# Kernel tuning notes

Measured on AMD Instinct MI355X. Metric: run time of the kernel, lower is better.

## Reference

```python
import jax, jax.numpy as jnp
import numpy as np

B, C, H, W, E, HEADS = 8, 128, 96, 96, 16, 4
HD = C // HEADS

def _ln(x, g, b, eps=1e-5):
    m = jnp.mean(x, axis=-1, keepdims=True)
    v = jnp.mean(jnp.square(x - m), axis=-1, keepdims=True)
    return (x - m) * jax.lax.rsqrt(v + eps) * g + b

def _gelu(x):
    return jax.nn.gelu(x, approximate=False)  # torch nn.GELU default (erf)

def setup_inputs() -> dict:
    key = jax.random.key(0)
    ks = iter(jax.random.split(key, 48))
    def wgt(shape, s=0.02):
        return jax.random.normal(next(ks), shape, jnp.float32) * s
    d = {
        "feature_map": jax.random.normal(next(ks), (B, C, H, W), jnp.float32),
        "hyperedge_scores": jax.random.uniform(next(ks), (B, H * W, E), jnp.float32),
        # norm_node_pre
        "np_g": jnp.ones((C,), jnp.float32), "np_b": jnp.zeros((C,), jnp.float32),
        # MultiheadAttention (self-attn over hyperedges)
        "mha_w_in": wgt((3 * C, C)), "mha_b_in": jnp.zeros((3 * C,), jnp.float32),
        "mha_w_out": wgt((C, C)), "mha_b_out": jnp.zeros((C,), jnp.float32),
        # transformer FFN
        "ffn_w1": wgt((2 * C, C)), "ffn_b1": jnp.zeros((2 * C,), jnp.float32),
        "ffn_w2": wgt((C, 2 * C)), "ffn_b2": jnp.zeros((C,), jnp.float32),
        # shared LayerNorm inside HypergraphTransformerConv (used twice)
        "tnorm_g": jnp.ones((C,), jnp.float32), "tnorm_b": jnp.zeros((C,), jnp.float32),
        # norm_hyper
        "nh_g": jnp.ones((C,), jnp.float32), "nh_b": jnp.zeros((C,), jnp.float32),
        # hyper_proj
        "hp_w": wgt((C, C)), "hp_b": jnp.zeros((C,), jnp.float32),
        # HyperedgeGuidedNodeAttention
        "q_w": wgt((C, C)), "q_b": jnp.zeros((C,), jnp.float32),
        "kv_w": wgt((2 * C, C)), "kv_b": jnp.zeros((2 * C,), jnp.float32),
        # norm_fusion
        "nf_g": jnp.ones((2 * C,), jnp.float32), "nf_b": jnp.zeros((2 * C,), jnp.float32),
        # gate = Linear(2C->C) + LayerNorm(C) + Sigmoid
        "gate_w": wgt((C, 2 * C)), "gate_b": jnp.zeros((C,), jnp.float32),
        "gate_ln_g": jnp.ones((C,), jnp.float32), "gate_ln_b": jnp.zeros((C,), jnp.float32),
        # node_proj
        "nproj_w": wgt((C, C)), "nproj_b": jnp.zeros((C,), jnp.float32),
    }
    return d

def _forward(feature_map, hyperedge_scores, np_g, np_b, mha_w_in, mha_b_in,
             mha_w_out, mha_b_out, ffn_w1, ffn_b1, ffn_w2, ffn_b2,
             tnorm_g, tnorm_b, nh_g, nh_b, hp_w, hp_b, q_w, q_b, kv_w, kv_b,
             nf_g, nf_b, gate_w, gate_b, gate_ln_g, gate_ln_b, nproj_w, nproj_b):
    b, c, h, w = feature_map.shape
    n = h * w
    node = jnp.transpose(feature_map.reshape(b, c, n), (0, 2, 1))   # [B,N,C]
    node = _ln(node, np_g, np_b)
    # hyperedge aggregation: H^T @ X -> [B,E,C]
    hyper = jnp.einsum('bne,bnc->bec', hyperedge_scores, node)
    # --- HypergraphTransformerConv (self-attn over E=16 hyperedges) ---
    qkv = hyper @ mha_w_in.T + mha_b_in                               # [B,E,3C]
    q, k, v = jnp.split(qkv, 3, axis=-1)
    def heads(x):  # [B,E,C] -> [B,h,E,hd]
        return jnp.transpose(x.reshape(b, E, HEADS, HD), (0, 2, 1, 3))
    q, k, v = heads(q), heads(k), heads(v)
    attn = jax.nn.softmax(jnp.einsum('bhqd,bhkd->bhqk', q, k) / np.sqrt(HD), axis=-1)
    ao = jnp.einsum('bhqk,bhkd->bhqd', attn, v)
    ao = jnp.transpose(ao, (0, 2, 1, 3)).reshape(b, E, c)
    ao = ao @ mha_w_out.T + mha_b_out
    x = _ln(hyper + ao, tnorm_g, tnorm_b)
    ffn = _gelu(x @ ffn_w1.T + ffn_b1) @ ffn_w2.T + ffn_b2
    hyper = _ln(x + ffn, tnorm_g, tnorm_b)
    # ---
    hyper = _ln(hyper, nh_g, nh_b)
    hyper = _gelu(hyper @ hp_w.T + hp_b)                              # [B,E,C]
    intra = jnp.einsum('bne,bec->bnc', hyperedge_scores, hyper)       # [B,N,C]
    # HyperedgeGuidedNodeAttention (scale = C**-0.5)
    Q = node @ q_w.T + q_b
    K, V = jnp.split(hyper @ kv_w.T + kv_b, 2, axis=-1)
    a = jax.nn.softmax(jnp.einsum('bnc,bec->bne', Q, K) * (c ** -0.5), axis=-1)
    cross = jnp.einsum('bne,bec->bnc', a, V)
    combined = _ln(jnp.concatenate([intra, cross], axis=-1), nf_g, nf_b)
    gate = jax.nn.sigmoid(_ln(combined @ gate_w.T + gate_b, gate_ln_g, gate_ln_b))
    fused = gate * intra + (1.0 - gate) * cross
    upd = node + fused                                                # dropout in eval mode
    out = _gelu(upd @ nproj_w.T + nproj_b)
    return jnp.transpose(out, (0, 2, 1)).reshape(b, c, h, w)

def reference(feature_map, hyperedge_scores, np_g, np_b, mha_w_in, mha_b_in,
              mha_w_out, mha_b_out, ffn_w1, ffn_b1, ffn_w2, ffn_b2,
              tnorm_g, tnorm_b, nh_g, nh_b, hp_w, hp_b, q_w, q_b, kv_w, kv_b,
              nf_g, nf_b, gate_w, gate_b, gate_ln_g, gate_ln_b, nproj_w, nproj_b):
    return _forward(feature_map, hyperedge_scores, np_g, np_b, mha_w_in, mha_b_in,
                    mha_w_out, mha_b_out, ffn_w1, ffn_b1, ffn_w2, ffn_b2,
                    tnorm_g, tnorm_b, nh_g, nh_b, hp_w, hp_b, q_w, q_b, kv_w, kv_b,
                    nf_g, nf_b, gate_w, gate_b, gate_ln_g, gate_ln_b, nproj_w, nproj_b)
```

## Files before the change

### kernel.cpp

```cpp
#include <hip/hip_runtime.h>

typedef unsigned short bf_t;
typedef unsigned int u32;
typedef short short8 __attribute__((ext_vector_type(8)));
typedef float f32x4 __attribute__((ext_vector_type(4)));

#define NB 8
#define CC 128
#define NN 9216
#define EE 16
#define NT 144
#define HS 24

__device__ __forceinline__ float b2f(bf_t u){ return __uint_as_float(((u32)u)<<16); }
__device__ __forceinline__ bf_t f2b(float f){
  u32 u = __float_as_uint(f);
  u = (u + 0x7fffu + ((u>>16)&1u)) >> 16;
  return (bf_t)u;
}
__device__ __forceinline__ float gelu_f(float x){ return 0.5f*x*(1.f+erff(x*0.70710678118654752f)); }
__device__ __forceinline__ float red16(float v){
  #pragma unroll
  for (int m=1;m<16;m<<=1) v += __shfl_xor(v, m, 16);
  return v;
}
__device__ __forceinline__ float grs(float var){
  return rsqrtf(fmaxf(var + 1e-5f, 1e-8f));
}
__device__ __forceinline__ short8 ldw8(const float* __restrict__ p){
  float4 a = *(const float4*)p;
  float4 b = *(const float4*)(p+4);
  short8 o;
  o[0]=(short)f2b(a.x); o[1]=(short)f2b(a.y); o[2]=(short)f2b(a.z); o[3]=(short)f2b(a.w);
  o[4]=(short)f2b(b.x); o[5]=(short)f2b(b.y); o[6]=(short)f2b(b.z); o[7]=(short)f2b(b.w);
  return o;
}

template<int MODE>
__global__ __launch_bounds__(256) void k_pre(float* __restrict__ hacc,
    const float* __restrict__ gw, const float* __restrict__ npw,
    bf_t* __restrict__ gwb, bf_t* __restrict__ npwb,
    const float* __restrict__ w_in, const float* __restrict__ w_out,
    const float* __restrict__ w1, const float* __restrict__ w2,
    const float* __restrict__ hpw, const float* __restrict__ kvw,
    const float* __restrict__ qw,
    bf_t* __restrict__ w_in_b, bf_t* __restrict__ w_out_b,
    bf_t* __restrict__ w1_b, bf_t* __restrict__ w2_b,
    bf_t* __restrict__ hpw_b, bf_t* __restrict__ kvw_b,
    bf_t* __restrict__ qwT_b){
  int i = blockIdx.x*256 + threadIdx.x;
  hacc[i] = 0.f;
  if (MODE >= 1){
    gwb[i]       = f2b(gw[i]);
    gwb[i+16384] = f2b(gw[i+16384]);
    npwb[i]      = f2b(npw[i]);
  }
  if (MODE == 2){
    #pragma unroll
    for (int k=0;k<3;k++) w_in_b[i + k*16384] = f2b(w_in[i + k*16384]);
    w_out_b[i]       = f2b(w_out[i]);
    w1_b[i]          = f2b(w1[i]);
    w1_b[i+16384]    = f2b(w1[i+16384]);
    w2_b[i]          = f2b(w2[i]);
    w2_b[i+16384]    = f2b(w2[i+16384]);
    hpw_b[i]         = f2b(hpw[i]);
    kvw_b[i]         = f2b(kvw[i]);
    kvw_b[i+16384]   = f2b(kvw[i+16384]);
    qwT_b[i]         = f2b(qw[(i&127)*128 + (i>>7)]);
  }
}

template<int BFOUT>
__global__ __launch_bounds__(256,4) void k_ln_agg(const float* __restrict__ fm,
                                                  const float* __restrict__ g,
                                                  const float* __restrict__ bb,
                                                  const float* __restrict__ sc,
                                                  float* __restrict__ nln,
                                                  bf_t* __restrict__ nlnb,
                                                  float* __restrict__ hacc){
  int b = blockIdx.y, n0 = blockIdx.x*64, tid = threadIdx.x;
  __shared__ float xs[128*65];
  __shared__ float scs[64][17];
  __shared__ float ps[4][64], pq[4][64], mrs[2][64];
  const float* base = fm + (size_t)b*CC*NN + n0;
  #pragma unroll
  for (int p=0;p<8;p++){
    int idx = tid + p*256;
    int c = idx>>4, n4 = (idx&15)*4;
    float4 v = *(const float4*)(base + (size_t)c*NN + n4);
    xs[c*65 + n4+0] = v.x; xs[c*65 + n4+1] = v.y;
    xs[c*65 + n4+2] = v.z; xs[c*65 + n4+3] = v.w;
  }
  { int n = tid>>2, e4 = (tid&3)*4;
    float4 sv = *(const float4*)(sc + ((size_t)(b*NN + n0 + n))*EE + e4);
    scs[n][e4+0] = sv.x; scs[n][e4+1] = sv.y;
    scs[n][e4+2] = sv.z; scs[n][e4+3] = sv.w;
  }
  __syncthreads();
  { int cg = tid>>6, n = tid&63;
    float s=0.f, q=0.f;
    #pragma unroll
    for (int c=0;c<32;c++){ float v = xs[(cg*32+c)*65 + n]; s+=v; q+=v*v; }
    ps[cg][n]=s; pq[cg][n]=q;
  }
  __syncthreads();
  if (tid < 64){
    float S = ps[0][tid]+ps[1][tid]+ps[2][tid]+ps[3][tid];
    float Q = pq[0][tid]+pq[1][tid]+pq[2][tid]+pq[3][tid];
    float m = S*(1.f/128.f);
    mrs[0][tid] = m; mrs[1][tid] = grs(Q*(1.f/128.f) - m*m);
  }
  __syncthreads();
  #pragma unroll
  for (int p=0;p<8;p++){
    int idx = tid + p*256;
    int c = idx>>4, n4 = (idx&15)*4;
    float gv = g[c], bv = bb[c];
    float v0 = (xs[c*65+n4+0]-mrs[0][n4+0])*mrs[1][n4+0]*gv + bv;
    float v1 = (xs[c*65+n4+1]-mrs[0][n4+1])*mrs[1][n4+1]*gv + bv;
    float v2 = (xs[c*65+n4+2]-mrs[0][n4+2])*mrs[1][n4+2]*gv + bv;
    float v3 = (xs[c*65+n4+3]-mrs[0][n4+3])*mrs[1][n4+3]*gv + bv;
    xs[c*65+n4+0]=v0; xs[c*65+n4+1]=v1; xs[c*65+n4+2]=v2; xs[c*65+n4+3]=v3;
    if (!BFOUT){
      float4 o; o.x=v0; o.y=v1; o.z=v2; o.w=v3;
      *(float4*)(nln + ((size_t)(b*CC + c))*NN + n0 + n4) = o;
    }
  }
  __syncthreads();
  if (BFOUT){
    #pragma unroll
    for (int p=0;p<4;p++){
      int idx = tid + p*256;
      int n = idx>>4, c8 = (idx&15)*8;
      short8 o;
      #pragma unroll
      for (int j=0;j<8;j++) o[j] = (short)f2b(xs[(c8+j)*65 + n]);
      *(short8*)(nlnb + ((size_t)(b*NN + n0 + n))*CC + c8) = o;
    }
  }
  { int cp = tid&63, eh = tid>>6;
    float a0[4]={0,0,0,0}, a1[4]={0,0,0,0};
    for (int n=0;n<64;n++){
      float x0 = xs[cp*65 + n], x1 = xs[(cp+64)*65 + n];
      #pragma unroll
      for (int j=0;j<4;j++){
        float se = scs[n][eh*4+j];
        a0[j] += se*x0; a1[j] += se*x1;
      }
    }
    #pragma unroll
    for (int j=0;j<4;j++){
      float* hb = hacc + (size_t)(b*EE + eh*4 + j)*CC;
      atomicAdd(hb + cp, a0[j]);
      atomicAdd(hb + cp + 64, a1[j]);
    }
  }
}

template<int K, int NOUT, int ACT, int WB, int NW>
__device__ __forceinline__ void gemm16(const bf_t* A, int SA,
                                       const float* __restrict__ W,
                                       const bf_t* __restrict__ Wb,
                                       const float* __restrict__ bias,
                                       bf_t* O, int SO, int tid){
  int lane = tid&63, wid = tid>>6;
  int m16 = lane&15, quad = lane>>4;
  for (int t0 = wid; t0 < NOUT/16; t0 += NW){
    int n0 = t0*16;
    f32x4 acc = {0.f,0.f,0.f,0.f};
    #pragma unroll
    for (int k0=0;k0<K;k0+=32){
      short8 af = *(const short8*)(A + m16*SA + k0 + quad*8);
      short8 bfv = WB ? *(const short8*)(Wb + (size_t)(n0+m16)*K + k0 + quad*8)
                      : ldw8(W + (size_t)(n0+m16)*K + k0 + quad*8);
      acc = __builtin_amdgcn_mfma_f32_16x16x32_bf16(af, bfv, acc, 0, 0, 0);
    }
    int col = n0 + m16;
    float bv = bias[col];
    #pragma unroll
    for (int r=0;r<4;r++){
      float v = acc[r] + bv;
      if (ACT) v = gelu_f(v);
      O[(quad*4+r)*SO + col] = f2b(v);
    }
  }
}

#define SP1 136
#define SP2 264
#define SP3 392

template<int WB>
__global__ __launch_bounds__(512) void k_edge(const float* __restrict__ hacc,
    const float* w_in, const float* b_in, const float* w_out, const float* b_out,
    const float* w1, const float* b1, const float* w2, const float* b2v,
    const float* tg, const float* tb, const float* nhg, const float* nhb,
    const float* hpw, const float* hpb, const float* kvw, const float* kvbias,
    const float* qw, const float* qb,
    const bf_t* __restrict__ w_in_b, const bf_t* __restrict__ w_out_b,
    const bf_t* __restrict__ w1_b, const bf_t* __restrict__ w2_b,
    const bf_t* __restrict__ hpw_b, const bf_t* __restrict__ kvw_b,
    const bf_t* __restrict__ qwT_b,
    bf_t* __restrict__ hfw, bf_t* __restrict__ vws,
    bf_t* __restrict__ Ktgb, float* __restrict__ qbK){
  __shared__ __align__(16) bf_t hyp0[16*SP1];
  __shared__ __align__(16) bf_t qkvb[16*SP3];
  __shared__ __align__(16) bf_t aob [16*SP1];
  __shared__ __align__(16) bf_t xnb [16*SP1];
  __shared__ __align__(16) bf_t h1b [16*SP2];
  __shared__ __align__(16) bf_t t2b [16*SP1];
  __shared__ __align__(16) bf_t hfb [16*SP1];
  __shared__ __align__(16) bf_t kvo [16*SP2];
  int b = blockIdx.x, tid = threadIdx.x;
  int lane = tid&63, wid = tid>>6, m16 = lane&15, quad = lane>>4;

  #pragma unroll
  for (int p=0;p<4;p++){
    int idx = tid + p*512;
    int e = idx>>7, c = idx&127;
    hyp0[e*SP1 + c] = f2b(hacc[(size_t)(b*EE + e)*CC + c]);
  }
  __syncthreads();
  gemm16<128,384,0,WB,8>(hyp0, SP1, w_in, w_in_b, b_in, qkvb, SP3, tid);
  __syncthreads();
  if (tid < 256){
    int part = tid&3, hq = tid>>2;
    int h = hq>>4, qi = hq&15;
    int dbase = h*32 + part*8;
    float qv[8];
    #pragma unroll
    for (int j=0;j<8;j++) qv[j] = b2f(qkvb[qi*SP3 + dbase + j]);
    float dot[16];
    #pragma unroll
    for (int kk=0;kk<16;kk++){
      float s = 0.f;
      #pragma unroll
      for (int j=0;j<8;j++) s += qv[j]*b2f(qkvb[kk*SP3 + 128 + dbase + j]);
      dot[kk] = s;
    }
    #pragma unroll
    for (int m=1;m<4;m<<=1){
      #pragma unroll
      for (int kk=0;kk<16;kk++) dot[kk] += __shfl_xor(dot[kk], m, 4);
    }
    const float sc1 = 0.17677669529663687f;
    float mx = -1e30f;
    #pragma unroll
    for (int kk=0;kk<16;kk++){ dot[kk] *= sc1; mx = fmaxf(mx, dot[kk]); }
    float sum = 0.f;
    #pragma unroll
    for (int kk=0;kk<16;kk++){ dot[kk] = __expf(dot[kk]-mx); sum += dot[kk]; }
    float inv = 1.f/sum;
    float ao[8] = {0,0,0,0,0,0,0,0};
    #pragma unroll
    for (int kk=0;kk<16;kk++){
      float p = dot[kk]*inv;
      #pragma unroll
      for (int j=0;j<8;j++) ao[j] += p*b2f(qkvb[kk*SP3 + 256 + dbase + j]);
    }
    #pragma unroll
    for (int j=0;j<8;j++) aob[qi*SP1 + dbase + j] = f2b(ao[j]);
  }
  __syncthreads();
  gemm16<128,128,0,WB,8>(aob, SP1, w_out, w_out_b, b_out, xnb, SP1, tid);
  __syncthreads();
  if (tid < 256){
    int e = tid>>4, i = tid&15;
    float v[8]; float s=0.f, q=0.f;
    #pragma unroll
    for (int j=0;j<8;j++){
      int c = i*8+j;
      v[j] = b2f(hyp0[e*SP1+c]) + b2f(xnb[e*SP1+c]);
      s += v[j]; q += v[j]*v[j];
    }
    s = red16(s); q = red16(q);
    float m = s*(1.f/128.f);
    float rs = grs(q*(1.f/128.f) - m*m);
    #pragma unroll
    for (int j=0;j<8;j++){
      int c = i*8+j;
      xnb[e*SP1+c] = f2b((v[j]-m)*rs*tg[c] + tb[c]);
    }
  }
  __syncthreads();
  gemm16<128,256,1,WB,8>(xnb, SP1, w1, w1_b, b1, h1b, SP2, tid);
  __syncthreads();
  gemm16<256,128,0,WB,8>(h1b, SP2, w2, w2_b, b2v, aob, SP1, tid);
  __syncthreads();
  if (tid < 256){
    int e = tid>>4, i = tid&15;
    float v[8]; float s=0.f, q=0.f;
    #pragma unroll
    for (int j=0;j<8;j++){
      int c = i*8+j;
      v[j] = b2f(xnb[e*SP1+c]) + b2f(aob[e*SP1+c]);
      s += v[j]; q += v[j]*v[j];
    }
    s = red16(s); q = red16(q);
    float m = s*(1.f/128.f);
    float rs = grs(q*(1.f/128.f) - m*m);
    float s2=0.f, q2=0.f;
    #pragma unroll
    for (int j=0;j<8;j++){
      int c = i*8+j;
      v[j] = (v[j]-m)*rs*tg[c] + tb[c];
      s2 += v[j]; q2 += v[j]*v[j];
    }
    s2 = red16(s2); q2 = red16(q2);
    float m2 = s2*(1.f/128.f);
    float rs2 = grs(q2*(1.f/128.f) - m2*m2);
    #pragma unroll
    for (int j=0;j<8;j++){
      int c = i*8+j;
      t2b[e*SP1+c] = f2b((v[j]-m2)*rs2*nhg[c] + nhb[c]);
    }
  }
  __syncthreads();
  gemm16<128,128,1,WB,8>(t2b, SP1, hpw, hpw_b, hpb, hfb, SP1, tid);
  __syncthreads();
  gemm16<128,256,0,WB,8>(hfb, SP1, kvw, kvw_b, kvbias, kvo, SP2, tid);
  __syncthreads();
  #pragma unroll
  for (int p=0;p<4;p++){
    int idx = tid + p*512;
    int e = idx>>7, c = idx&127;
    size_t o = (size_t)(b*EE + e)*CC + c;
    hfw[o] = hfb[e*SP1 + c];
    vws[o] = kvo[e*SP2 + 128 + c];
  }
  {
    int n0 = wid*16;
    f32x4 acc = {0.f,0.f,0.f,0.f};
    #pragma unroll
    for (int k0=0;k0<128;k0+=32){
      short8 a = *(const short8*)(kvo + m16*SP2 + k0 + quad*8);
      short8 bq;
      if (WB){
        bq = *(const short8*)(qwT_b + (size_t)(n0+m16)*128 + k0 + quad*8);
      } else {
        #pragma unroll
        for (int j=0;j<8;j++)
          bq[j] = (short)f2b(qw[(size_t)(k0+quad*8+j)*128 + n0+m16]);
      }
      acc = __builtin_amdgcn_mfma_f32_16x16x32_bf16(a, bq, acc, 0, 0, 0);
    }
    #pragma unroll
    for (int r=0;r<4;r++)
      Ktgb[(size_t)(b*EE + quad*4 + r)*CC + n0 + m16] = f2b(acc[r]);
  }
  if (tid < 256){
    int e = tid>>4, i = tid&15;
    float s = 0.f;
    #pragma unroll
    for (int j=0;j<8;j++) s += qb[i*8+j]*b2f(kvo[e*SP2 + i*8+j]);
    s = red16(s);
    if (i == 0) qbK[b*EE + e] = s;
  }
}

template<int MODE>
__global__ __launch_bounds__(256,3) void k_meganode(
    float* __restrict__ io, const bf_t* __restrict__ nlnb,
    const float* __restrict__ sc,
    const bf_t* __restrict__ hf, const bf_t* __restrict__ vw,
    const bf_t* __restrict__ ktg, const float* __restrict__ qbK,
    const float* __restrict__ nfg, const float* __restrict__ nfb,
    const float* __restrict__ gw, const bf_t* __restrict__ gwb,
    const float* __restrict__ gb,
    const float* __restrict__ glng, const float* __restrict__ glnb,
    const float* __restrict__ npw, const bf_t* __restrict__ npwb,
    const float* __restrict__ npb){
  int tid = threadIdx.x, lane = tid&63, wid = tid>>6;
  int m16 = lane&15, quad = lane>>4;
  int b = blockIdx.y, n0 = blockIdx.x*64;
  __shared__ __align__(16) char sm[37120];
  bf_t* xt  = (bf_t*)(sm);
  bf_t* ktT = (bf_t*)(sm + 17408);
  bf_t* hfT = (bf_t*)(sm + 21760);
  bf_t* vfT = (bf_t*)(sm + 27904);
  bf_t* ash = (bf_t*)(sm + 34048);
  bf_t* ct  = (bf_t*)(sm + 17408);
  const short8 z8 = {0,0,0,0,0,0,0,0};

  if (MODE == 2){
    const bf_t* nb = nlnb + ((size_t)(b*NN + n0))*CC;
    #pragma unroll
    for (int p=0;p<4;p++){
      int idx = tid + p*256;
      int n = idx>>4, c8 = (idx&15)*8;
      *(short8*)&xt[n*136 + c8] = *(const short8*)(nb + (size_t)n*CC + c8);
    }
  } else {
    #pragma unroll
    for (int p=0;p<8;p++){
      int idx = tid + p*256;
      int c = idx>>4, n4 = (idx&15)*4;
      float4 v = *(const float4*)(io + ((size_t)(b*CC + c))*NN + n0 + n4);
      xt[(n4+0)*136 + c] = f2b(v.x);
      xt[(n4+1)*136 + c] = f2b(v.y);
      xt[(n4+2)*136 + c] = f2b(v.z);
      xt[(n4+3)*136 + c] = f2b(v.w);
    }
  }
  { const u32* kp = (const u32*)(ktg + (size_t)b*EE*CC);
    #pragma unroll
    for (int p=0;p<4;p++){
      int idx = tid + p*256;
      int e = idx>>6, c2 = (idx&63)*2;
      *(u32*)&ktT[e*136 + c2] = kp[idx];
    }
  }
  { const u32* hs = (const u32*)(hf + (size_t)b*EE*CC);
    const u32* vs = (const u32*)(vw + (size_t)b*EE*CC);
    #pragma unroll
    for (int p=0;p<4;p++){
      int idx = tid + p*256;
      int e = idx>>6, c2 = (idx&63)*2;
      u32 hv = hs[idx], vv = vs[idx];
      hfT[(c2+0)*HS + e] = (bf_t)(hv&0xffffu);
      hfT[(c2+1)*HS + e] = (bf_t)(hv>>16);
      vfT[(c2+0)*HS + e] = (bf_t)(vv&0xffffu);
      vfT[(c2+1)*HS + e] = (bf_t)(vv>>16);
    }
  }
  __syncthreads();

  f32x4 dacc = {0.f,0.f,0.f,0.f};
  #pragma unroll
  for (int kk=0;kk<4;kk++){
    short8 a = *(const short8*)(xt + (wid*16+m16)*136 + kk*32 + quad*8);
    short8 bfr = *(const short8*)(ktT + m16*136 + kk*32 + quad*8);
    dacc = __builtin_amdgcn_mfma_f32_16x16x32_bf16(a, bfr, dacc, 0, 0, 0);
  }
  { float qbe = qbK[b*EE + m16];
    #pragma unroll
    for (int r=0;r<4;r++){
      float v = (dacc[r] + qbe) * 0.08838834764831845f;
      float m = v;
      #pragma unroll
      for (int msk=1;msk<16;msk<<=1) m = fmaxf(m, __shfl_xor(m, msk, 16));
      float ex = __expf(v - m);
      float s = ex;
      #pragma unroll
      for (int msk=1;msk<16;msk<<=1) s += __shfl_xor(s, msk, 16);
      ash[(wid*16 + quad*4 + r)*HS + m16] = f2b(ex / s);
    }
  }

  short8 scf = z8, asf = z8;
  if (quad < 2){
    const float* sp = sc + ((size_t)(b*NN + n0 + wid*16 + m16))*EE + quad*8;
    float4 u0 = *(const float4*)sp;
    float4 u1 = *(const float4*)(sp+4);
    scf[0]=(short)f2b(u0.x); scf[1]=(short)f2b(u0.y); scf[2]=(short)f2b(u0.z); scf[3]=(short)f2b(u0.w);
    scf[4]=(short)f2b(u1.x); scf[5]=(short)f2b(u1.y); scf[6]=(short)f2b(u1.z); scf[7]=(short)f2b(u1.w);
    asf = *(const short8*)(ash + (wid*16+m16)*HS + quad*8);
  }
  f32x4 acc_it[8], acc_cr[8];
  #pragma unroll
  for (int t=0;t<8;t++){
    short8 bh = z8, bv = z8;
    if (quad < 2){
      bh = *(const short8*)(hfT + (t*16+m16)*HS + quad*8);
      bv = *(const short8*)(vfT + (t*16+m16)*HS + quad*8);
    }
    f32x4 zf = {0.f,0.f,0.f,0.f};
    acc_it[t] = __builtin_amdgcn_mfma_f32_16x16x32_bf16(scf, bh, zf, 0, 0, 0);
    acc_cr[t] = __builtin_amdgcn_mfma_f32_16x16x32_bf16(asf, bv, zf, 0, 0, 0);
  }

  float mean4[4], rstd4[4];
  { float s4[4]={0,0,0,0}, q4[4]={0,0,0,0};
    #pragma unroll
    for (int t=0;t<8;t++)
      #pragma unroll
      for (int r=0;r<4;r++){
        float a = acc_it[t][r], c = acc_cr[t][r];
        s4[r] += a + c; q4[r] += a*a + c*c;
      }
    #pragma unroll
    for (int r=0;r<4;r++){
      s4[r] = red16(s4[r]); q4[r] = red16(q4[r]);
      mean4[r] = s4[r]*(1.f/256.f);
      rstd4[r] = grs(q4[r]*(1.f/256.f) - mean4[r]*mean4[r]);
    }
  }
  __syncthreads();
  short8 af[8];
  #pragma unroll
  for (int s=0;s<2;s++){
    #pragma unroll
    for (int r=0;r<4;r++){
      int node = wid*16 + quad*4 + r;
      #pragma unroll
      for (int t=0;t<4;t++){
        int ch = (s*4+t)*16 + m16;
        ct[node*72 + t*16 + m16] = f2b((acc_it[s*4+t][r]-mean4[r])*rstd4[r]*nfg[ch] + nfb[ch]);
      }
    }
    #pragma unroll
    for (int k2=0;k2<2;k2++)
      af[s*2+k2] = *(const short8*)(ct + (wid*16+m16)*72 + k2*32 + quad*8);
  }
  #pragma unroll
  for (int s=0;s<2;s++){
    #pragma unroll
    for (int r=0;r<4;r++){
      int node = wid*16 + quad*4 + r;
      #pragma unroll
      for (int t=0;t<4;t++){
        int ch = (s*4+t)*16 + m16;
        ct[node*72 + t*16 + m16] = f2b((acc_cr[s*4+t][r]-mean4[r])*rstd4[r]*nfg[128+ch] + nfb[128+ch]);
      }
    }
    #pragma unroll
    for (int k2=0;k2<2;k2++)
      af[4+s*2+k2] = *(const short8*)(ct + (wid*16+m16)*72 + k2*32 + quad*8);
  }

  f32x4 acc_g[8];
  #pragma unroll
  for (int t=0;t<8;t++){
    f32x4 a = {0.f,0.f,0.f,0.f};
    #pragma unroll
    for (int kk=0;kk<8;kk++){
      short8 w8 = (MODE >= 1) ? *(const short8*)(gwb + (size_t)(t*16+m16)*256 + kk*32 + quad*8)
                              : ldw8(gw + (size_t)(t*16+m16)*256 + kk*32 + quad*8);
      a = __builtin_amdgcn_mfma_f32_16x16x32_bf16(af[kk], w8, a, 0, 0, 0);
    }
    acc_g[t] = a;
  }

  { float s2[4]={0,0,0,0}, q2[4]={0,0,0,0};
    #pragma unroll
    for (int t=0;t<8;t++){
      float bv = gb[t*16+m16];
      #pragma unroll
      for (int r=0;r<4;r++){
        float v = acc_g[t][r] + bv;
        acc_g[t][r] = v; s2[r] += v; q2[r] += v*v;
      }
    }
    float m2r[4], rs2r[4];
    #pragma unroll
    for (int r=0;r<4;r++){
      s2[r] = red16(s2[r]); q2[r] = red16(q2[r]);
      m2r[r] = s2[r]*(1.f/128.f);
      rs2r[r] = grs(q2[r]*(1.f/128.f) - m2r[r]*m2r[r]);
    }
    #pragma unroll
    for (int t=0;t<8;t++){
      int col = t*16 + m16;
      float lg = glng[col], lb = glnb[col];
      #pragma unroll
      for (int r=0;r<4;r++){
        float z = (acc_g[t][r]-m2r[r])*rs2r[r]*lg + lb;
        float gs = 1.f/(1.f + __expf(-z));
        int node = wid*16 + quad*4 + r;
        float nld = b2f(xt[node*136 + col]);
        xt[node*136 + col] = f2b(nld + gs*acc_it[t][r] + (1.f-gs)*acc_cr[t][r]);
      }
    }
  }

  short8 bfu[4];
  #pragma unroll
  for (int kk=0;kk<4;kk++)
    bfu[kk] = *(const short8*)(xt + (wid*16+m16)*136 + kk*32 + quad*8);
  #pragma unroll
  for (int mt=0;mt<8;mt++){
    f32x4 o = {0.f,0.f,0.f,0.f};
    #pragma unroll
    for (int kk=0;kk<4;kk++){
      short8 aw = (MODE >= 1) ? *(const short8*)(npwb + (size_t)(mt*16+m16)*128 + kk*32 + quad*8)
                              : ldw8(npw + (size_t)(mt*16+m16)*128 + kk*32 + quad*8);
      o = __builtin_amdgcn_mfma_f32_16x16x32_bf16(aw, bfu[kk], o, 0, 0, 0);
    }
    #pragma unroll
    for (int r=0;r<4;r++){
      int cp = mt*16 + quad*4 + r;
      io[((size_t)(b*CC + cp))*NN + n0 + wid*16 + m16] = gelu_f(o[r] + npb[cp]);
    }
  }
}

extern "C" void kernel_launch(void* const* d_in, const int* in_sizes, int n_in,
                              void* d_out, int out_size, void* d_ws, size_t ws_size,
                              hipStream_t stream){
  (void)in_sizes; (void)n_in; (void)out_size;
  const float* fm   = (const float*)d_in[0];
  const float* sc   = (const float*)d_in[1];
  const float* npg  = (const float*)d_in[2];
  const float* npb_ = (const float*)d_in[3];
  const float* w_in = (const float*)d_in[4];
  const float* b_in = (const float*)d_in[5];
  const float* w_out= (const float*)d_in[6];
  const float* b_out= (const float*)d_in[7];
  const float* w1   = (const float*)d_in[8];
  const float* b1   = (const float*)d_in[9];
  const float* w2   = (const float*)d_in[10];
  const float* b2v  = (const float*)d_in[11];
  const float* tg   = (const float*)d_in[12];
  const float* tb   = (const float*)d_in[13];
  const float* nhg  = (const float*)d_in[14];
  const float* nhb  = (const float*)d_in[15];
  const float* hpw  = (const float*)d_in[16];
  const float* hpb  = (const float*)d_in[17];
  const float* qw   = (const float*)d_in[18];
  const float* qb   = (const float*)d_in[19];
  const float* kvw  = (const float*)d_in[20];
  const float* kvb  = (const float*)d_in[21];
  const float* nfg  = (const float*)d_in[22];
  const float* nfb  = (const float*)d_in[23];
  const float* gw   = (const float*)d_in[24];
  const float* gb   = (const float*)d_in[25];
  const float* glng = (const float*)d_in[26];
  const float* glnb = (const float*)d_in[27];
  const float* npw  = (const float*)d_in[28];
  const float* npb2 = (const float*)d_in[29];

  float* nln = (float*)d_out;

  char* w = (char*)d_ws;
  float* hacc    = (float*)(w);
  float* qbK     = (float*)(w + 65536);
  bf_t*  hfw     = (bf_t*) (w + 66048);
  bf_t*  vws     = (bf_t*) (w + 98816);
  bf_t*  Ktgb    = (bf_t*) (w + 131584);
  bf_t*  gwb     = (bf_t*) (w + 164352);
  bf_t*  npwb    = (bf_t*) (w + 229888);
  bf_t*  w_in_b  = (bf_t*) (w + 262656);
  bf_t*  w_out_b = (bf_t*) (w + 360960);
  bf_t*  w1_b    = (bf_t*) (w + 393728);
  bf_t*  w2_b    = (bf_t*) (w + 459264);
  bf_t*  hpw_b   = (bf_t*) (w + 524800);
  bf_t*  kvw_b   = (bf_t*) (w + 557568);
  bf_t*  qwT_b   = (bf_t*) (w + 623104);
  bf_t*  nlnb    = (bf_t*) (w + 655872);
  bool full  = (ws_size >= (size_t)19530240);
  bool pre   = (ws_size >= (size_t)262656);

  if (full){
    k_pre<2><<<dim3(64), dim3(256), 0, stream>>>(hacc, gw, npw, gwb, npwb,
        w_in, w_out, w1, w2, hpw, kvw, qw,
        w_in_b, w_out_b, w1_b, w2_b, hpw_b, kvw_b, qwT_b);
    k_ln_agg<1><<<dim3(NT,8), dim3(256), 0, stream>>>(fm, npg, npb_, sc, nln, nlnb, hacc);
    k_edge<1><<<dim3(8), dim3(512), 0, stream>>>(hacc, w_in,b_in,w_out,b_out,
        w1,b1,w2,b2v, tg,tb, nhg,nhb, hpw,hpb, kvw,kvb, qw,qb,
        w_in_b, w_out_b, w1_b, w2_b, hpw_b, kvw_b, qwT_b,
        hfw, vws, Ktgb, qbK);
    k_meganode<2><<<dim3(NT,8), dim3(256), 0, stream>>>(nln, nlnb, sc, hfw, vws, Ktgb, qbK,
        nfg, nfb, gw, gwb, gb, glng, glnb, npw, npwb, npb2);
  } else if (pre){
    k_pre<1><<<dim3(64), dim3(256), 0, stream>>>(hacc, gw, npw, gwb, npwb,
        w_in, w_out, w1, w2, hpw, kvw, qw,
        w_in_b, w_out_b, w1_b, w2_b, hpw_b, kvw_b, qwT_b);
    k_ln_agg<0><<<dim3(NT,8), dim3(256), 0, stream>>>(fm, npg, npb_, sc, nln, nlnb, hacc);
    k_edge<0><<<dim3(8), dim3(512), 0, stream>>>(hacc, w_in,b_in,w_out,b_out,
        w1,b1,w2,b2v, tg,tb, nhg,nhb, hpw,hpb, kvw,kvb, qw,qb,
        w_in_b, w_out_b, w1_b, w2_b, hpw_b, kvw_b, qwT_b,
        hfw, vws, Ktgb, qbK);
    k_meganode<1><<<dim3(NT,8), dim3(256), 0, stream>>>(nln, nlnb, sc, hfw, vws, Ktgb, qbK,
        nfg, nfb, gw, gwb, gb, glng, glnb, npw, npwb, npb2);
  } else {
    k_pre<0><<<dim3(64), dim3(256), 0, stream>>>(hacc, gw, npw, gwb, npwb,
        w_in, w_out, w1, w2, hpw, kvw, qw,
        w_in_b, w_out_b, w1_b, w2_b, hpw_b, kvw_b, qwT_b);
    k_ln_agg<0><<<dim3(NT,8), dim3(256), 0, stream>>>(fm, npg, npb_, sc, nln, nlnb, hacc);
    k_edge<0><<<dim3(8), dim3(512), 0, stream>>>(hacc, w_in,b_in,w_out,b_out,
        w1,b1,w2,b2v, tg,tb, nhg,nhb, hpw,hpb, kvw,kvb, qw,qb,
        w_in_b, w_out_b, w1_b, w2_b, hpw_b, kvw_b, qwT_b,
        hfw, vws, Ktgb, qbK);
    k_meganode<0><<<dim3(NT,8), dim3(256), 0, stream>>>(nln, nlnb, sc, hfw, vws, Ktgb, qbK,
        nfg, nfb, gw, gwb, gb, glng, glnb, npw, npwb, npb2);
  }
}
```

Measured before the change: 261.3 us.

## Split hyperedge aggregation out of LayerNorm kernel into separate reduction kernel

In the full-workspace path, the LN kernel no longer computes the score-weighted aggregation; a new kernel reads the bf16 normalized nodes and scores back from global memory. Each block covers 256 nodes instead of 64, which cuts atomic adds per batch by four and shortens the LN kernel's serial 64-node loop. It costs an extra launch and re-reading the bf16 node buffer. Aggregation now uses bf16-rounded activations, a small precision change.

```diff
diff --git a/kernel.cpp b/kernel.cpp
--- a/kernel.cpp
+++ b/kernel.cpp
@@ -70,7 +70,7 @@
   }
 }
 
-template<int BFOUT>
+template<int BFOUT, int AGG>
 __global__ __launch_bounds__(256,4) void k_ln_agg(const float* __restrict__ fm,
                                                   const float* __restrict__ g,
                                                   const float* __restrict__ bb,
@@ -91,7 +91,8 @@
     xs[c*65 + n4+0] = v.x; xs[c*65 + n4+1] = v.y;
     xs[c*65 + n4+2] = v.z; xs[c*65 + n4+3] = v.w;
   }
-  { int n = tid>>2, e4 = (tid&3)*4;
+  if (AGG){
+    int n = tid>>2, e4 = (tid&3)*4;
     float4 sv = *(const float4*)(sc + ((size_t)(b*NN + n0 + n))*EE + e4);
     scs[n][e4+0] = sv.x; scs[n][e4+1] = sv.y;
     scs[n][e4+2] = sv.z; scs[n][e4+3] = sv.w;
@@ -138,7 +139,8 @@
       *(short8*)(nlnb + ((size_t)(b*NN + n0 + n))*CC + c8) = o;
     }
   }
-  { int cp = tid&63, eh = tid>>6;
+  if (AGG){
+    int cp = tid&63, eh = tid>>6;
     float a0[4]={0,0,0,0}, a1[4]={0,0,0,0};
     for (int n=0;n<64;n++){
       float x0 = xs[cp*65 + n], x1 = xs[(cp+64)*65 + n];
@@ -155,6 +157,27 @@
       atomicAdd(hb + cp + 64, a1[j]);
     }
   }
+}
+
+__global__ __launch_bounds__(512) void k_agg(const bf_t* __restrict__ nlnb,
+                                             const float* __restrict__ sc,
+                                             float* __restrict__ hacc){
+  int b = blockIdx.y, n0 = blockIdx.x*256, tid = threadIdx.x;
+  int cp = tid & 127, eg = tid >> 7;
+  const bf_t* nb = nlnb + ((size_t)(b*NN + n0))*CC + cp;
+  const float* sp = sc + ((size_t)(b*NN + n0))*EE + eg*4;
+  float a0=0.f, a1=0.f, a2=0.f, a3=0.f;
+  #pragma unroll 4
+  for (int n=0;n<256;n++){
+    float nv = b2f(nb[(size_t)n*CC]);
+    float4 sv = *(const float4*)(sp + (size_t)n*EE);
+    a0 += sv.x*nv; a1 += sv.y*nv; a2 += sv.z*nv; a3 += sv.w*nv;
+  }
+  float* hb = hacc + (size_t)(b*EE + eg*4)*CC + cp;
+  atomicAdd(hb,        a0);
+  atomicAdd(hb + CC,   a1);
+  atomicAdd(hb + 2*CC, a2);
+  atomicAdd(hb + 3*CC, a3);
 }
 
 template<int K, int NOUT, int ACT, int WB, int NW>
@@ -644,7 +667,8 @@
     k_pre<2><<<dim3(64), dim3(256), 0, stream>>>(hacc, gw, npw, gwb, npwb,
         w_in, w_out, w1, w2, hpw, kvw, qw,
         w_in_b, w_out_b, w1_b, w2_b, hpw_b, kvw_b, qwT_b);
-    k_ln_agg<1><<<dim3(NT,8), dim3(256), 0, stream>>>(fm, npg, npb_, sc, nln, nlnb, hacc);
+    k_ln_agg<1,0><<<dim3(NT,8), dim3(256), 0, stream>>>(fm, npg, npb_, sc, nln, nlnb, hacc);
+    k_agg<<<dim3(36,8), dim3(512), 0, stream>>>(nlnb, sc, hacc);
     k_edge<1><<<dim3(8), dim3(512), 0, stream>>>(hacc, w_in,b_in,w_out,b_out,
         w1,b1,w2,b2v, tg,tb, nhg,nhb, hpw,hpb, kvw,kvb, qw,qb,
         w_in_b, w_out_b, w1_b, w2_b, hpw_b, kvw_b, qwT_b,
@@ -655,7 +679,7 @@
     k_pre<1><<<dim3(64), dim3(256), 0, stream>>>(hacc, gw, npw, gwb, npwb,
         w_in, w_out, w1, w2, hpw, kvw, qw,
         w_in_b, w_out_b, w1_b, w2_b, hpw_b, kvw_b, qwT_b);
-    k_ln_agg<0><<<dim3(NT,8), dim3(256), 0, stream>>>(fm, npg, npb_, sc, nln, nlnb, hacc);
+    k_ln_agg<0,1><<<dim3(NT,8), dim3(256), 0, stream>>>(fm, npg, npb_, sc, nln, nlnb, hacc);
     k_edge<0><<<dim3(8), dim3(512), 0, stream>>>(hacc, w_in,b_in,w_out,b_out,
         w1,b1,w2,b2v, tg,tb, nhg,nhb, hpw,hpb, kvw,kvb, qw,qb,
         w_in_b, w_out_b, w1_b, w2_b, hpw_b, kvw_b, qwT_b,
@@ -666,7 +690,7 @@
     k_pre<0><<<dim3(64), dim3(256), 0, stream>>>(hacc, gw, npw, gwb, npwb,
         w_in, w_out, w1, w2, hpw, kvw, qw,
         w_in_b, w_out_b, w1_b, w2_b, hpw_b, kvw_b, qwT_b);
-    k_ln_agg<0><<<dim3(NT,8), dim3(256), 0, stream>>>(fm, npg, npb_, sc, nln, nlnb, hacc);
+    k_ln_agg<0,1><<<dim3(NT,8), dim3(256), 0, stream>>>(fm, npg, npb_, sc, nln, nlnb, hacc);
     k_edge<0><<<dim3(8), dim3(512), 0, stream>>>(hacc, w_in,b_in,w_out,b_out,
         w1,b1,w2,b2v, tg,tb, nhg,nhb, hpw,hpb, kvw,kvb, qw,qb,
         w_in_b, w_out_b, w1_b, w2_b, hpw_b, kvw_b, qwT_b,
```

Result: slower. 290.1 us (+11.0%).
